# Kernel tuning notes

Hardware: AMD Instinct MI355X
Metric: run time of the kernel (lower is better)

Reference implementation:

```python
import jax, jax.numpy as jnp
import numpy as np

N_NODES = 100000


def gcn_layer(x, src, dst, W, b, num_nodes):
    """PyG GCNConv: out = D^-1/2 (A + I) D^-1/2 (x W) + b, with self-loops."""
    h = x @ W  # [N, out_dim]
    # add self-loops
    loop = jnp.arange(num_nodes, dtype=src.dtype)
    s = jnp.concatenate([src, loop])
    d = jnp.concatenate([dst, loop])
    # symmetric normalization (degree counted on destination, incl. self-loops)
    deg = jax.ops.segment_sum(jnp.ones_like(d, dtype=h.dtype), d, num_segments=num_nodes)
    dinv = jnp.where(deg > 0, jax.lax.rsqrt(deg), 0.0)
    norm = dinv[s] * dinv[d]  # [E+N]
    # gather -> weight -> scatter-add
    msg = h[s] * norm[:, None]  # [E+N, out_dim]
    out = jax.ops.segment_sum(msg, d, num_segments=num_nodes)
    return out + b


def setup_inputs() -> dict:
    key = jax.random.key(0)
    k1, k2, k3, k4 = jax.random.split(key, 4)
    in_chan, h1, h2 = 256, 128, 64
    n_edges = 1600000
    x = jax.random.normal(k1, (N_NODES, in_chan), dtype=jnp.float32)
    edge_index = jax.random.randint(k2, (2, n_edges), 0, N_NODES, dtype=jnp.int64)
    W1 = jax.random.normal(k3, (in_chan, h1), dtype=jnp.float32) * (1.0 / np.sqrt(in_chan))
    b1 = jnp.zeros((h1,), dtype=jnp.float32)
    W2 = jax.random.normal(k4, (h1, h2), dtype=jnp.float32) * (1.0 / np.sqrt(h1))
    b2 = jnp.zeros((h2,), dtype=jnp.float32)
    return {"x": x, "edge_index": edge_index, "W1": W1, "b1": b1, "W2": W2, "b2": b2}


def reference(x, edge_index, W1, b1, W2, b2):
    src, dst = edge_index[0], edge_index[1]
    h = jax.nn.relu(gcn_layer(x, src, dst, W1, b1, N_NODES))
    return jax.nn.relu(gcn_layer(h, src, dst, W2, b2, N_NODES))
```

## Files before the change

### kernel.cpp

```cpp
#include <hip/hip_runtime.h>
#include <hip/hip_fp16.h>

#define NNODES 100000

#define OFF_W1TH     0UL
#define OFF_W1TL     65536UL
#define OFF_W2TH     131072UL
#define OFF_W2TL     147456UL
#define OFF_BCNT     163840UL
#define OFF_BBASE    165888UL
#define OFF_BCUR     167936UL
#define OFF_ROWPTR   400128UL
#define OFF_DINV     1200640UL
#define OFF_COL      1605632UL
#define OFF_EBUF     8005632UL
#define OFF_H1G      8005632UL
#define OFF_H1OUT    59205632UL

typedef __attribute__((ext_vector_type(8))) _Float16 f16x8;
typedef __attribute__((ext_vector_type(4))) float f32x4;

__device__ __forceinline__ void async_copy16(void* lds, const void* g) {
    __builtin_amdgcn_global_load_lds(
        (const __attribute__((address_space(1))) unsigned*)g,
        (__attribute__((address_space(3))) unsigned*)lds, 16, 0, 0);
}

__global__ __launch_bounds__(256) void bincount(const int* __restrict__ dst,
                                                int* __restrict__ bcnt, int E) {
    __shared__ int lc[512];
    int t = threadIdx.x;
    lc[t] = 0; lc[t + 256] = 0;
    __syncthreads();
    for (int e = blockIdx.x * 256 + t; e < E; e += gridDim.x * 256)
        atomicAdd(&lc[dst[e] >> 8], 1);
    __syncthreads();
    if (lc[t]) atomicAdd(&bcnt[t], lc[t]);
    if (lc[t + 256]) atomicAdd(&bcnt[t + 256], lc[t + 256]);
}

__global__ __launch_bounds__(512) void bscan(const int* __restrict__ bcnt,
                                             int* __restrict__ bbase,
                                             int* __restrict__ bcur,
                                             int* __restrict__ rowptr,
                                             int NB, int N, int E) {
    __shared__ int s[512];
    int t = threadIdx.x;
    int v = (t < NB) ? bcnt[t] : 0;
    s[t] = v;
    __syncthreads();
    for (int off = 1; off < 512; off <<= 1) {
        int add = (t >= off) ? s[t - off] : 0;
        __syncthreads();
        s[t] += add;
        __syncthreads();
    }
    if (t < NB) {
        int ex = s[t] - v;
        bbase[t] = ex;
        bcur[t] = ex;
    }
    if (t == 0) rowptr[N] = E;
}

#define CHUNK 8192
__global__ __launch_bounds__(256) void binscatter(const int* __restrict__ src,
                                                  const int* __restrict__ dst,
                                                  int* __restrict__ bcur,
                                                  int* __restrict__ ebuf, int E) {
    __shared__ int lc[512];
    __shared__ int gb[512];
    int t = threadIdx.x;
    lc[t] = 0; lc[t + 256] = 0;
    __syncthreads();
    int base = blockIdx.x * CHUNK;
    int rb[32];
#pragma unroll
    for (int i = 0; i < 32; ++i) {
        int e = base + i * 256 + t;
        if (e < E) {
            int b = dst[e] >> 8;
            rb[i] = (b << 13) | atomicAdd(&lc[b], 1);
        } else rb[i] = -1;
    }
    __syncthreads();
    if (lc[t]) gb[t] = atomicAdd(&bcur[t], lc[t]);
    if (lc[t + 256]) gb[t + 256] = atomicAdd(&bcur[t + 256], lc[t + 256]);
    __syncthreads();
#pragma unroll
    for (int i = 0; i < 32; ++i) {
        if (rb[i] >= 0) {
            int e = base + i * 256 + t;
            int b = rb[i] >> 13, r = rb[i] & 8191;
            ebuf[gb[b] + r] = src[e] | ((dst[e] & 255) << 20);
        }
    }
}

__global__ __launch_bounds__(256) void buildcsr(const int* __restrict__ ebuf,
                                                const int* __restrict__ bbase,
                                                const int* __restrict__ bcnt,
                                                int* __restrict__ rowptr,
                                                int* __restrict__ colarr,
                                                float* __restrict__ dinv, int N) {
    int b = blockIdx.x;
    int t = threadIdx.x;
    int start = bbase[b];
    int cnt = bcnt[b];
    __shared__ int nc[256];
    __shared__ int s[256];
    __shared__ int ncur[256];
    nc[t] = 0;
    __syncthreads();
    for (int e = t; e < cnt; e += 256) atomicAdd(&nc[ebuf[start + e] >> 20], 1);
    __syncthreads();
    int own = nc[t];
    s[t] = own;
    __syncthreads();
    for (int off = 1; off < 256; off <<= 1) {
        int add = (t >= off) ? s[t - off] : 0;
        __syncthreads();
        s[t] += add;
        __syncthreads();
    }
    int rowbase = start + s[t] - own;
    int n0 = b << 8;
    if (n0 + t < N) {
        rowptr[n0 + t] = rowbase;
        dinv[n0 + t] = rsqrtf((float)(own + 1));
    }
    ncur[t] = rowbase;
    __syncthreads();
    for (int e = t; e < cnt; e += 256) {
        int pe = ebuf[start + e];
        int slot = atomicAdd(&ncur[pe >> 20], 1);
        colarr[slot] = pe & 0xFFFFF;
    }
}

__global__ __launch_bounds__(256) void split_wt_frag(const float* __restrict__ W,
                                                     _Float16* __restrict__ hi,
                                                     _Float16* __restrict__ lo,
                                                     int K, int N) {
    int idx = blockIdx.x * 256 + threadIdx.x;
    if (idx >= K * N) return;
    int NT = N >> 4;
    int j = idx & 7;
    int l = (idx >> 3) & 63;
    int f = idx >> 9;
    int nt = f % NT;
    int kc = f / NT;
    int k = kc * 32 + (l >> 4) * 8 + j;
    int n = nt * 16 + (l & 15);
    float v = W[k * N + n];
    _Float16 h = (_Float16)v;
    hi[idx] = h;
    lo[idx] = (_Float16)(v - (float)h);
}

template <int BN, int KTOT, bool AFP16>
__global__ __launch_bounds__(256, 3) void gemm_f16(const void* __restrict__ Araw,
                                                   const _Float16* __restrict__ Bh_g,
                                                   const _Float16* __restrict__ Bl_g,
                                                   const float* __restrict__ dinv,
                                                   _Float16* __restrict__ C, int M) {
    constexpr int NT = BN / 16;
    constexpr int FPW = (2 * NT) / 4;
    __shared__ _Float16 Ah[128][72];
    __shared__ _Float16 Bsh[2 * NT * 512];
    __shared__ _Float16 Bsl[2 * NT * 512];

    const int tid = threadIdx.x;
    const int wave = tid >> 6;
    const int lane = tid & 63;
    const int lm = lane & 15;
    const int q = lane >> 4;
    const int m0 = blockIdx.x * 128;

    f32x4 acc[2][NT];
#pragma unroll
    for (int a = 0; a < 2; ++a)
#pragma unroll
        for (int b = 0; b < NT; ++b) acc[a][b] = (f32x4){0.f, 0.f, 0.f, 0.f};

    for (int k0 = 0; k0 < KTOT; k0 += 64) {
        const int kc0 = k0 >> 5;
        const _Float16* bh_base = Bh_g + (size_t)kc0 * NT * 512;
        const _Float16* bl_base = Bl_g + (size_t)kc0 * NT * 512;
#pragma unroll
        for (int i = 0; i < FPW; ++i) {
            int f = wave * FPW + i;
            async_copy16(&Bsh[f * 512 + lane * 8], bh_base + f * 512 + lane * 8);
            async_copy16(&Bsl[f * 512 + lane * 8], bl_base + f * 512 + lane * 8);
        }
#pragma unroll
        for (int i = 0; i < 4; ++i) {
            int flat = tid + i * 256;
            int row = flat >> 3;
            int kk = (flat & 7) << 3;
            int gr = m0 + row;
            if (AFP16) {
                uint4 hv = make_uint4(0u, 0u, 0u, 0u);
                if (gr < M)
                    hv = *(const uint4*)&((const _Float16*)Araw)[(size_t)gr * KTOT + k0 + kk];
                *(uint4*)&Ah[row][kk] = hv;
            } else {
                const float* Af = (const float*)Araw;
                float4 v0 = make_float4(0.f, 0.f, 0.f, 0.f);
                float4 v1 = make_float4(0.f, 0.f, 0.f, 0.f);
                if (gr < M) {
                    v0 = *(const float4*)&Af[(size_t)gr * KTOT + k0 + kk];
                    v1 = *(const float4*)&Af[(size_t)gr * KTOT + k0 + kk + 4];
                }
                f16x8 h;
                h[0] = (_Float16)v0.x; h[1] = (_Float16)v0.y;
                h[2] = (_Float16)v0.z; h[3] = (_Float16)v0.w;
                h[4] = (_Float16)v1.x; h[5] = (_Float16)v1.y;
                h[6] = (_Float16)v1.z; h[7] = (_Float16)v1.w;
                *(f16x8*)&Ah[row][kk] = h;
            }
        }
        __syncthreads();

#pragma unroll
        for (int dkc = 0; dkc < 2; ++dkc) {
            f16x8 a[2];
#pragma unroll
            for (int mt = 0; mt < 2; ++mt)
                a[mt] = *(const f16x8*)&Ah[wave * 32 + mt * 16 + lm][dkc * 32 + q * 8];
#pragma unroll
            for (int nt = 0; nt < NT; ++nt) {
                f16x8 bh = *(const f16x8*)&Bsh[(dkc * NT + nt) * 512 + lane * 8];
                f16x8 bl = *(const f16x8*)&Bsl[(dkc * NT + nt) * 512 + lane * 8];
#pragma unroll
                for (int mt = 0; mt < 2; ++mt) {
                    acc[mt][nt] = __builtin_amdgcn_mfma_f32_16x16x32_f16(a[mt], bh, acc[mt][nt], 0, 0, 0);
                    acc[mt][nt] = __builtin_amdgcn_mfma_f32_16x16x32_f16(a[mt], bl, acc[mt][nt], 0, 0, 0);
                }
            }
        }
        __syncthreads();
    }

#pragma unroll
    for (int mt = 0; mt < 2; ++mt) {
#pragma unroll
        for (int i = 0; i < 4; ++i) {
            int r = m0 + wave * 32 + mt * 16 + q * 4 + i;
            if (r < M) {
                float dv = dinv[r];
#pragma unroll
                for (int nt = 0; nt < NT; ++nt) {
                    C[(size_t)r * BN + nt * 16 + lm] = (_Float16)(acc[mt][nt][i] * dv);
                }
            }
        }
    }
}

__device__ __forceinline__ void acc8(float* a, uint4 v) {
    float2 f0 = __half22float2(*(const __half2*)&v.x);
    float2 f1 = __half22float2(*(const __half2*)&v.y);
    float2 f2 = __half22float2(*(const __half2*)&v.z);
    float2 f3 = __half22float2(*(const __half2*)&v.w);
    a[0] += f0.x; a[1] += f0.y; a[2] += f1.x; a[3] += f1.y;
    a[4] += f2.x; a[5] += f2.y; a[6] += f3.x; a[7] += f3.y;
}

__global__ __launch_bounds__(256) void agg128(const _Float16* __restrict__ g,
                                              const int* __restrict__ rowptr,
                                              const int* __restrict__ colarr,
                                              const float* __restrict__ dinv,
                                              const float* __restrict__ bias,
                                              _Float16* __restrict__ out, int n) {
    int node = blockIdx.x * 4 + (threadIdx.x >> 6);
    int lane = threadIdx.x & 63;
    if (node >= n) return;
    int sel = lane >> 4;
    int co = (lane & 15) << 3;

    int beg = rowptr[node];
    int end = rowptr[node + 1];

    float a[8] = {0.f, 0.f, 0.f, 0.f, 0.f, 0.f, 0.f, 0.f};
    if (sel == 0) acc8(a, *(const uint4*)&g[(node << 7) + co]);

    int p = beg;
    for (; p + 16 <= end; p += 16) {
        int r0 = colarr[p + sel];
        int r1 = colarr[p + 4 + sel];
        int r2 = colarr[p + 8 + sel];
        int r3 = colarr[p + 12 + sel];
        uint4 v0 = *(const uint4*)&g[(r0 << 7) + co];
        uint4 v1 = *(const uint4*)&g[(r1 << 7) + co];
        uint4 v2 = *(const uint4*)&g[(r2 << 7) + co];
        uint4 v3 = *(const uint4*)&g[(r3 << 7) + co];
        acc8(a, v0); acc8(a, v1); acc8(a, v2); acc8(a, v3);
    }
    for (; p + 4 <= end; p += 4) {
        int r = colarr[p + sel];
        acc8(a, *(const uint4*)&g[(r << 7) + co]);
    }
    int rem = end - p;
    if (sel < rem) {
        int r = colarr[p + sel];
        acc8(a, *(const uint4*)&g[(r << 7) + co]);
    }

#pragma unroll
    for (int i = 0; i < 8; ++i) {
        a[i] += __shfl(a[i], lane ^ 16);
        a[i] += __shfl(a[i], lane ^ 32);
    }

    if (sel == 0) {
        float dv = dinv[node];
        float4 b0 = *(const float4*)&bias[co];
        float4 b1 = *(const float4*)&bias[co + 4];
        float o0 = fmaxf(fmaf(a[0], dv, b0.x), 0.f);
        float o1 = fmaxf(fmaf(a[1], dv, b0.y), 0.f);
        float o2 = fmaxf(fmaf(a[2], dv, b0.z), 0.f);
        float o3 = fmaxf(fmaf(a[3], dv, b0.w), 0.f);
        float o4 = fmaxf(fmaf(a[4], dv, b1.x), 0.f);
        float o5 = fmaxf(fmaf(a[5], dv, b1.y), 0.f);
        float o6 = fmaxf(fmaf(a[6], dv, b1.z), 0.f);
        float o7 = fmaxf(fmaf(a[7], dv, b1.w), 0.f);
        __half2 h0 = __floats2half2_rn(o0, o1);
        __half2 h1 = __floats2half2_rn(o2, o3);
        __half2 h2 = __floats2half2_rn(o4, o5);
        __half2 h3 = __floats2half2_rn(o6, o7);
        uint4 pk = make_uint4(*(unsigned*)&h0, *(unsigned*)&h1,
                              *(unsigned*)&h2, *(unsigned*)&h3);
        *(uint4*)&out[(node << 7) + co] = pk;
    }
}

__global__ __launch_bounds__(256) void agg64(const _Float16* __restrict__ g,
                                             const int* __restrict__ rowptr,
                                             const int* __restrict__ colarr,
                                             const float* __restrict__ dinv,
                                             const float* __restrict__ bias,
                                             float* __restrict__ out, int n) {
    int node = blockIdx.x * 4 + (threadIdx.x >> 6);
    int lane = threadIdx.x & 63;
    if (node >= n) return;
    int sel = lane >> 3;
    int co = (lane & 7) << 3;

    int beg = rowptr[node];
    int end = rowptr[node + 1];

    float a[8] = {0.f, 0.f, 0.f, 0.f, 0.f, 0.f, 0.f, 0.f};
    if (sel == 0) acc8(a, *(const uint4*)&g[(node << 6) + co]);

    int p = beg;
    for (; p + 16 <= end; p += 16) {
        int r0 = colarr[p + sel];
        int r1 = colarr[p + 8 + sel];
        uint4 v0 = *(const uint4*)&g[(r0 << 6) + co];
        uint4 v1 = *(const uint4*)&g[(r1 << 6) + co];
        acc8(a, v0); acc8(a, v1);
    }
    for (; p + 8 <= end; p += 8) {
        int r = colarr[p + sel];
        acc8(a, *(const uint4*)&g[(r << 6) + co]);
    }
    int rem = end - p;
    if (sel < rem) {
        int r = colarr[p + sel];
        acc8(a, *(const uint4*)&g[(r << 6) + co]);
    }

#pragma unroll
    for (int i = 0; i < 8; ++i) {
        a[i] += __shfl(a[i], lane ^ 8);
        a[i] += __shfl(a[i], lane ^ 16);
        a[i] += __shfl(a[i], lane ^ 32);
    }

    if (sel == 0) {
        float dv = dinv[node];
        float4 b0 = *(const float4*)&bias[co];
        float4 b1 = *(const float4*)&bias[co + 4];
        float4 oA, oB;
        oA.x = fmaxf(fmaf(a[0], dv, b0.x), 0.f);
        oA.y = fmaxf(fmaf(a[1], dv, b0.y), 0.f);
        oA.z = fmaxf(fmaf(a[2], dv, b0.z), 0.f);
        oA.w = fmaxf(fmaf(a[3], dv, b0.w), 0.f);
        oB.x = fmaxf(fmaf(a[4], dv, b1.x), 0.f);
        oB.y = fmaxf(fmaf(a[5], dv, b1.y), 0.f);
        oB.z = fmaxf(fmaf(a[6], dv, b1.z), 0.f);
        oB.w = fmaxf(fmaf(a[7], dv, b1.w), 0.f);
        *(float4*)&out[(node << 6) + co] = oA;
        *(float4*)&out[(node << 6) + co + 4] = oB;
    }
}

extern "C" void kernel_launch(void* const* d_in, const int* in_sizes, int n_in,
                              void* d_out, int out_size, void* d_ws, size_t ws_size,
                              hipStream_t stream) {
    const float* x  = (const float*)d_in[0];
    const int*   ei = (const int*)d_in[1];
    const float* W1 = (const float*)d_in[2];
    const float* b1 = (const float*)d_in[3];
    const float* W2 = (const float*)d_in[4];
    const float* b2 = (const float*)d_in[5];
    float* out = (float*)d_out;

    const int E = in_sizes[1] / 2;
    const int H1 = in_sizes[3];
    const int K1 = in_sizes[2] / H1;
    const int N = in_sizes[0] / K1;
    const int H2 = in_sizes[4] / H1;
    const int* src = ei;
    const int* dst = ei + E;
    const int NB = (N + 255) >> 8;

    char* ws = (char*)d_ws;
    _Float16* w1th   = (_Float16*)(ws + OFF_W1TH);
    _Float16* w1tl   = (_Float16*)(ws + OFF_W1TL);
    _Float16* w2th   = (_Float16*)(ws + OFF_W2TH);
    _Float16* w2tl   = (_Float16*)(ws + OFF_W2TL);
    int*      bcnt   = (int*)(ws + OFF_BCNT);
    int*      bbase  = (int*)(ws + OFF_BBASE);
    int*      bcur   = (int*)(ws + OFF_BCUR);
    int*      rowptr = (int*)(ws + OFF_ROWPTR);
    float*    dinv   = (float*)(ws + OFF_DINV);
    int*      colarr = (int*)(ws + OFF_COL);
    int*      ebuf   = (int*)(ws + OFF_EBUF);
    _Float16* h1g    = (_Float16*)(ws + OFF_H1G);
    _Float16* h1out  = (_Float16*)(ws + OFF_H1OUT);
    _Float16* h2g    = (_Float16*)(ws + OFF_H1G);

    hipMemsetAsync(bcnt, 0, 512 * sizeof(int), stream);
    bincount<<<256, 256, 0, stream>>>(dst, bcnt, E);
    bscan<<<1, 512, 0, stream>>>(bcnt, bbase, bcur, rowptr, NB, N, E);
    binscatter<<<(E + CHUNK - 1) / CHUNK, 256, 0, stream>>>(src, dst, bcur, ebuf, E);
    buildcsr<<<NB, 256, 0, stream>>>(ebuf, bbase, bcnt, rowptr, colarr, dinv, N);

    split_wt_frag<<<(K1 * H1 + 255) / 256, 256, 0, stream>>>(W1, w1th, w1tl, K1, H1);
    split_wt_frag<<<(H1 * H2 + 255) / 256, 256, 0, stream>>>(W2, w2th, w2tl, H1, H2);

    gemm_f16<128, 256, false><<<(N + 127) / 128, 256, 0, stream>>>(x, w1th, w1tl, dinv, h1g, N);
    agg128<<<(N + 3) / 4, 256, 0, stream>>>(h1g, rowptr, colarr, dinv, b1, h1out, N);

    gemm_f16<64, 128, true><<<(N + 127) / 128, 256, 0, stream>>>(h1out, w2th, w2tl, dinv, h2g, N);
    agg64<<<(N + 3) / 4, 256, 0, stream>>>(h2g, rowptr, colarr, dinv, b2, out, N);
}
```

Before: 372.7 us.

## Double-buffer B tiles and load A fragments directly into registers in GEMM

Restructures the dense GEMM so the split-fp16 weight tiles are double-buffered in LDS with async copies for the next K chunk issued before the current chunk's MFMAs. The A operand is no longer staged through LDS. Each lane loads its own fragment straight from global memory into registers, prefetched one chunk ahead. Launch bounds are raised to 4 blocks per CU. This removes the LDS round-trip and one barrier per step and overlaps loads with math, but lanes now read A in scattered 16/32-byte pieces with less coalescing, and register pressure goes up.

```diff
diff --git a/kernel.cpp b/kernel.cpp
--- a/kernel.cpp
+++ b/kernel.cpp
@@ -159,16 +159,17 @@
 }
 
 template <int BN, int KTOT, bool AFP16>
-__global__ __launch_bounds__(256, 3) void gemm_f16(const void* __restrict__ Araw,
+__global__ __launch_bounds__(256, 4) void gemm_f16(const void* __restrict__ Araw,
                                                    const _Float16* __restrict__ Bh_g,
                                                    const _Float16* __restrict__ Bl_g,
                                                    const float* __restrict__ dinv,
                                                    _Float16* __restrict__ C, int M) {
     constexpr int NT = BN / 16;
-    constexpr int FPW = (2 * NT) / 4;
-    __shared__ _Float16 Ah[128][72];
-    __shared__ _Float16 Bsh[2 * NT * 512];
-    __shared__ _Float16 Bsl[2 * NT * 512];
+    constexpr int NK = KTOT / 32;
+    constexpr int TILE = NT * 512;
+    constexpr int FPW = NT / 4;
+    __shared__ _Float16 Bsh[2][TILE];
+    __shared__ _Float16 Bsl[2][TILE];
 
     const int tid = threadIdx.x;
     const int wave = tid >> 6;
@@ -177,70 +178,90 @@
     const int q = lane >> 4;
     const int m0 = blockIdx.x * 128;
 
+    const int r0 = m0 + wave * 32 + lm;
+    const int r1 = r0 + 16;
+    const bool vr0 = r0 < M;
+    const bool vr1 = r1 < M;
+
+    const float* Af = (const float*)Araw;
+    const _Float16* Ah16 = (const _Float16*)Araw;
+
     f32x4 acc[2][NT];
 #pragma unroll
     for (int a = 0; a < 2; ++a)
 #pragma unroll
         for (int b = 0; b < NT; ++b) acc[a][b] = (f32x4){0.f, 0.f, 0.f, 0.f};
 
-    for (int k0 = 0; k0 < KTOT; k0 += 64) {
-        const int kc0 = k0 >> 5;
-        const _Float16* bh_base = Bh_g + (size_t)kc0 * NT * 512;
-        const _Float16* bl_base = Bl_g + (size_t)kc0 * NT * 512;
-#pragma unroll
-        for (int i = 0; i < FPW; ++i) {
-            int f = wave * FPW + i;
-            async_copy16(&Bsh[f * 512 + lane * 8], bh_base + f * 512 + lane * 8);
-            async_copy16(&Bsl[f * 512 + lane * 8], bl_base + f * 512 + lane * 8);
+    float4 pa0, pa1, pa2, pa3;
+    uint4 ph0, ph1;
+
+#define STAGE_B(kc_, b_)                                                          \
+    do {                                                                          \
+        _Pragma("unroll")                                                         \
+        for (int i_ = 0; i_ < FPW; ++i_) {                                        \
+            int f_ = wave * FPW + i_;                                             \
+            async_copy16(&Bsh[b_][f_ * 512 + lane * 8],                           \
+                         Bh_g + (size_t)(kc_) * TILE + f_ * 512 + lane * 8);      \
+            async_copy16(&Bsl[b_][f_ * 512 + lane * 8],                           \
+                         Bl_g + (size_t)(kc_) * TILE + f_ * 512 + lane * 8);      \
+        }                                                                         \
+    } while (0)
+
+#define LOAD_A(t_)                                                                \
+    do {                                                                          \
+        const int k_ = (t_) * 32 + q * 8;                                         \
+        if (AFP16) {                                                              \
+            ph0 = vr0 ? *(const uint4*)&Ah16[(size_t)r0 * KTOT + k_]              \
+                      : make_uint4(0u, 0u, 0u, 0u);                               \
+            ph1 = vr1 ? *(const uint4*)&Ah16[(size_t)r1 * KTOT + k_]              \
+                      : make_uint4(0u, 0u, 0u, 0u);                               \
+        } else {                                                                  \
+            float4 z_ = make_float4(0.f, 0.f, 0.f, 0.f);                          \
+            pa0 = vr0 ? *(const float4*)&Af[(size_t)r0 * KTOT + k_] : z_;         \
+            pa1 = vr0 ? *(const float4*)&Af[(size_t)r0 * KTOT + k_ + 4] : z_;     \
+            pa2 = vr1 ? *(const float4*)&Af[(size_t)r1 * KTOT + k_] : z_;         \
+            pa3 = vr1 ? *(const float4*)&Af[(size_t)r1 * KTOT + k_ + 4] : z_;     \
+        }                                                                         \
+    } while (0)
+
+    STAGE_B(0, 0);
+    LOAD_A(0);
+    __syncthreads();
+
+#pragma unroll
+    for (int t = 0; t < NK; ++t) {
+        const int b = t & 1;
+        if (t + 1 < NK) STAGE_B(t + 1, b ^ 1);
+
+        f16x8 a0, a1;
+        if (AFP16) {
+            a0 = *(f16x8*)&ph0;
+            a1 = *(f16x8*)&ph1;
+        } else {
+            a0[0] = (_Float16)pa0.x; a0[1] = (_Float16)pa0.y;
+            a0[2] = (_Float16)pa0.z; a0[3] = (_Float16)pa0.w;
+            a0[4] = (_Float16)pa1.x; a0[5] = (_Float16)pa1.y;
+            a0[6] = (_Float16)pa1.z; a0[7] = (_Float16)pa1.w;
+            a1[0] = (_Float16)pa2.x; a1[1] = (_Float16)pa2.y;
+            a1[2] = (_Float16)pa2.z; a1[3] = (_Float16)pa2.w;
+            a1[4] = (_Float16)pa3.x; a1[5] = (_Float16)pa3.y;
+            a1[6] = (_Float16)pa3.z; a1[7] = (_Float16)pa3.w;
         }
-#pragma unroll
-        for (int i = 0; i < 4; ++i) {
-            int flat = tid + i * 256;
-            int row = flat >> 3;
-            int kk = (flat & 7) << 3;
-            int gr = m0 + row;
-            if (AFP16) {
-                uint4 hv = make_uint4(0u, 0u, 0u, 0u);
-                if (gr < M)
-                    hv = *(const uint4*)&((const _Float16*)Araw)[(size_t)gr * KTOT + k0 + kk];
-                *(uint4*)&Ah[row][kk] = hv;
-            } else {
-                const float* Af = (const float*)Araw;
-                float4 v0 = make_float4(0.f, 0.f, 0.f, 0.f);
-                float4 v1 = make_float4(0.f, 0.f, 0.f, 0.f);
-                if (gr < M) {
-                    v0 = *(const float4*)&Af[(size_t)gr * KTOT + k0 + kk];
-                    v1 = *(const float4*)&Af[(size_t)gr * KTOT + k0 + kk + 4];
-                }
-                f16x8 h;
-                h[0] = (_Float16)v0.x; h[1] = (_Float16)v0.y;
-                h[2] = (_Float16)v0.z; h[3] = (_Float16)v0.w;
-                h[4] = (_Float16)v1.x; h[5] = (_Float16)v1.y;
-                h[6] = (_Float16)v1.z; h[7] = (_Float16)v1.w;
-                *(f16x8*)&Ah[row][kk] = h;
-            }
+        if (t + 1 < NK) LOAD_A(t + 1);
+
+#pragma unroll
+        for (int nt = 0; nt < NT; ++nt) {
+            f16x8 bh = *(const f16x8*)&Bsh[b][nt * 512 + lane * 8];
+            f16x8 bl = *(const f16x8*)&Bsl[b][nt * 512 + lane * 8];
+            acc[0][nt] = __builtin_amdgcn_mfma_f32_16x16x32_f16(a0, bh, acc[0][nt], 0, 0, 0);
+            acc[0][nt] = __builtin_amdgcn_mfma_f32_16x16x32_f16(a0, bl, acc[0][nt], 0, 0, 0);
+            acc[1][nt] = __builtin_amdgcn_mfma_f32_16x16x32_f16(a1, bh, acc[1][nt], 0, 0, 0);
+            acc[1][nt] = __builtin_amdgcn_mfma_f32_16x16x32_f16(a1, bl, acc[1][nt], 0, 0, 0);
         }
-        __syncthreads();
-
-#pragma unroll
-        for (int dkc = 0; dkc < 2; ++dkc) {
-            f16x8 a[2];
-#pragma unroll
-            for (int mt = 0; mt < 2; ++mt)
-                a[mt] = *(const f16x8*)&Ah[wave * 32 + mt * 16 + lm][dkc * 32 + q * 8];
-#pragma unroll
-            for (int nt = 0; nt < NT; ++nt) {
-                f16x8 bh = *(const f16x8*)&Bsh[(dkc * NT + nt) * 512 + lane * 8];
-                f16x8 bl = *(const f16x8*)&Bsl[(dkc * NT + nt) * 512 + lane * 8];
-#pragma unroll
-                for (int mt = 0; mt < 2; ++mt) {
-                    acc[mt][nt] = __builtin_amdgcn_mfma_f32_16x16x32_f16(a[mt], bh, acc[mt][nt], 0, 0, 0);
-                    acc[mt][nt] = __builtin_amdgcn_mfma_f32_16x16x32_f16(a[mt], bl, acc[mt][nt], 0, 0, 0);
-                }
-            }
-        }
-        __syncthreads();
-    }
+        if (t + 1 < NK) __syncthreads();
+    }
+#undef STAGE_B
+#undef LOAD_A
 
 #pragma unroll
     for (int mt = 0; mt < 2; ++mt) {
```

Result: slower. 417.5 us (+12.0%).

## Double-buffer A tile in GEMM with register prefetch of next K phase

Applied to the files above, without the earlier changes.

The GEMM now loads the next 64-wide K slice of A into registers while MFMAs run on the current slice, then converts it into a second LDS buffer. The K loop is fully unrolled and launch bounds drop from 3 to 2 blocks per SM to make room for the extra registers and LDS. The goal is to hide global load latency behind compute. The cost is lower occupancy and an extra barrier per phase around the B staging, since B stays single-buffered.

```diff
diff --git a/kernel.cpp b/kernel.cpp
--- a/kernel.cpp
+++ b/kernel.cpp
@@ -159,14 +159,15 @@
 }
 
 template <int BN, int KTOT, bool AFP16>
-__global__ __launch_bounds__(256, 3) void gemm_f16(const void* __restrict__ Araw,
+__global__ __launch_bounds__(256, 2) void gemm_f16(const void* __restrict__ Araw,
                                                    const _Float16* __restrict__ Bh_g,
                                                    const _Float16* __restrict__ Bl_g,
                                                    const float* __restrict__ dinv,
                                                    _Float16* __restrict__ C, int M) {
     constexpr int NT = BN / 16;
+    constexpr int NPH = KTOT / 64;
     constexpr int FPW = (2 * NT) / 4;
-    __shared__ _Float16 Ah[128][72];
+    __shared__ _Float16 Ah[2][128][72];
     __shared__ _Float16 Bsh[2 * NT * 512];
     __shared__ _Float16 Bsl[2 * NT * 512];
 
@@ -177,57 +178,92 @@
     const int q = lane >> 4;
     const int m0 = blockIdx.x * 128;
 
+    const float* Af = (const float*)Araw;
+    const _Float16* Ah16 = (const _Float16*)Araw;
+
     f32x4 acc[2][NT];
 #pragma unroll
     for (int a = 0; a < 2; ++a)
 #pragma unroll
         for (int b = 0; b < NT; ++b) acc[a][b] = (f32x4){0.f, 0.f, 0.f, 0.f};
 
-    for (int k0 = 0; k0 < KTOT; k0 += 64) {
-        const int kc0 = k0 >> 5;
-        const _Float16* bh_base = Bh_g + (size_t)kc0 * NT * 512;
-        const _Float16* bl_base = Bl_g + (size_t)kc0 * NT * 512;
-#pragma unroll
-        for (int i = 0; i < FPW; ++i) {
-            int f = wave * FPW + i;
-            async_copy16(&Bsh[f * 512 + lane * 8], bh_base + f * 512 + lane * 8);
-            async_copy16(&Bsl[f * 512 + lane * 8], bl_base + f * 512 + lane * 8);
-        }
-#pragma unroll
-        for (int i = 0; i < 4; ++i) {
-            int flat = tid + i * 256;
-            int row = flat >> 3;
-            int kk = (flat & 7) << 3;
-            int gr = m0 + row;
-            if (AFP16) {
-                uint4 hv = make_uint4(0u, 0u, 0u, 0u);
-                if (gr < M)
-                    hv = *(const uint4*)&((const _Float16*)Araw)[(size_t)gr * KTOT + k0 + kk];
-                *(uint4*)&Ah[row][kk] = hv;
-            } else {
-                const float* Af = (const float*)Araw;
-                float4 v0 = make_float4(0.f, 0.f, 0.f, 0.f);
-                float4 v1 = make_float4(0.f, 0.f, 0.f, 0.f);
-                if (gr < M) {
-                    v0 = *(const float4*)&Af[(size_t)gr * KTOT + k0 + kk];
-                    v1 = *(const float4*)&Af[(size_t)gr * KTOT + k0 + kk + 4];
-                }
-                f16x8 h;
-                h[0] = (_Float16)v0.x; h[1] = (_Float16)v0.y;
-                h[2] = (_Float16)v0.z; h[3] = (_Float16)v0.w;
-                h[4] = (_Float16)v1.x; h[5] = (_Float16)v1.y;
-                h[6] = (_Float16)v1.z; h[7] = (_Float16)v1.w;
-                *(f16x8*)&Ah[row][kk] = h;
-            }
-        }
-        __syncthreads();
+    const float4 fz_ = make_float4(0.f, 0.f, 0.f, 0.f);
+    const uint4 uz_ = make_uint4(0u, 0u, 0u, 0u);
+
+    float4 va[4][2];
+    uint4 ua[4];
+
+#define AISSUE(t_)                                                                \
+    do {                                                                          \
+        _Pragma("unroll")                                                         \
+        for (int i = 0; i < 4; ++i) {                                             \
+            int flat = tid + i * 256;                                             \
+            int row = flat >> 3;                                                  \
+            int kk = (flat & 7) << 3;                                             \
+            int gr = m0 + row;                                                    \
+            int gk = (t_) * 64 + kk;                                              \
+            if (AFP16) {                                                          \
+                ua[i] = (gr < M) ? *(const uint4*)&Ah16[(size_t)gr * KTOT + gk]   \
+                                 : uz_;                                           \
+            } else {                                                              \
+                va[i][0] = (gr < M) ? *(const float4*)&Af[(size_t)gr * KTOT + gk] \
+                                    : fz_;                                        \
+                va[i][1] = (gr < M)                                               \
+                               ? *(const float4*)&Af[(size_t)gr * KTOT + gk + 4]  \
+                               : fz_;                                             \
+            }                                                                     \
+        }                                                                         \
+    } while (0)
+
+#define ACVT(buf_)                                                                \
+    do {                                                                          \
+        _Pragma("unroll")                                                         \
+        for (int i = 0; i < 4; ++i) {                                             \
+            int flat = tid + i * 256;                                             \
+            int row = flat >> 3;                                                  \
+            int kk = (flat & 7) << 3;                                             \
+            if (AFP16) {                                                          \
+                *(uint4*)&Ah[buf_][row][kk] = ua[i];                              \
+            } else {                                                              \
+                f16x8 h;                                                          \
+                h[0] = (_Float16)va[i][0].x; h[1] = (_Float16)va[i][0].y;         \
+                h[2] = (_Float16)va[i][0].z; h[3] = (_Float16)va[i][0].w;         \
+                h[4] = (_Float16)va[i][1].x; h[5] = (_Float16)va[i][1].y;         \
+                h[6] = (_Float16)va[i][1].z; h[7] = (_Float16)va[i][1].w;         \
+                *(f16x8*)&Ah[buf_][row][kk] = h;                                  \
+            }                                                                     \
+        }                                                                         \
+    } while (0)
+
+#define STAGE_B(t_)                                                               \
+    do {                                                                          \
+        const int kc0_ = (t_) * 2;                                                \
+        const _Float16* bh_ = Bh_g + (size_t)kc0_ * NT * 512;                     \
+        const _Float16* bl_ = Bl_g + (size_t)kc0_ * NT * 512;                     \
+        _Pragma("unroll")                                                         \
+        for (int i = 0; i < FPW; ++i) {                                           \
+            int f_ = wave * FPW + i;                                              \
+            async_copy16(&Bsh[f_ * 512 + lane * 8], bh_ + f_ * 512 + lane * 8);   \
+            async_copy16(&Bsl[f_ * 512 + lane * 8], bl_ + f_ * 512 + lane * 8);   \
+        }                                                                         \
+    } while (0)
+
+    AISSUE(0);
+    ACVT(0);
+    STAGE_B(0);
+    __syncthreads();
+
+    int cur = 0;
+#pragma unroll
+    for (int t = 0; t < NPH; ++t) {
+        if (t + 1 < NPH) AISSUE(t + 1);
 
 #pragma unroll
         for (int dkc = 0; dkc < 2; ++dkc) {
             f16x8 a[2];
 #pragma unroll
             for (int mt = 0; mt < 2; ++mt)
-                a[mt] = *(const f16x8*)&Ah[wave * 32 + mt * 16 + lm][dkc * 32 + q * 8];
+                a[mt] = *(const f16x8*)&Ah[cur][wave * 32 + mt * 16 + lm][dkc * 32 + q * 8];
 #pragma unroll
             for (int nt = 0; nt < NT; ++nt) {
                 f16x8 bh = *(const f16x8*)&Bsh[(dkc * NT + nt) * 512 + lane * 8];
@@ -239,8 +275,18 @@
                 }
             }
         }
-        __syncthreads();
-    }
+
+        if (t + 1 < NPH) {
+            ACVT(cur ^ 1);
+            __syncthreads();
+            STAGE_B(t + 1);
+            __syncthreads();
+            cur ^= 1;
+        }
+    }
+#undef AISSUE
+#undef ACVT
+#undef STAGE_B
 
 #pragma unroll
     for (int mt = 0; mt < 2; ++mt) {
```

New measurement: 424.0 us. +13.8%, slower.

## Stage full A tile once and double-buffer B weight tiles in GEMM

Applied to the files above, without the earlier changes.

The GEMM now loads the whole 128-row A tile across all of K into LDS up front, with a padded stride, instead of reloading per 64-wide K step. The fp16 hi/lo weight tiles are double-buffered, so the next phase's async copy overlaps the current phase's MFMAs, and the per-step barriers drop to one per phase. The occupancy hint of 3 is removed from launch bounds. LDS use grows considerably, which may lower occupancy on the 256-wide K layer.

```diff
diff --git a/kernel.cpp b/kernel.cpp
--- a/kernel.cpp
+++ b/kernel.cpp
@@ -159,16 +159,21 @@
 }
 
 template <int BN, int KTOT, bool AFP16>
-__global__ __launch_bounds__(256, 3) void gemm_f16(const void* __restrict__ Araw,
-                                                   const _Float16* __restrict__ Bh_g,
-                                                   const _Float16* __restrict__ Bl_g,
-                                                   const float* __restrict__ dinv,
-                                                   _Float16* __restrict__ C, int M) {
+__global__ __launch_bounds__(256) void gemm_f16(const void* __restrict__ Araw,
+                                                const _Float16* __restrict__ Bh_g,
+                                                const _Float16* __restrict__ Bl_g,
+                                                const float* __restrict__ dinv,
+                                                _Float16* __restrict__ C, int M) {
     constexpr int NT = BN / 16;
-    constexpr int FPW = (2 * NT) / 4;
-    __shared__ _Float16 Ah[128][72];
-    __shared__ _Float16 Bsh[2 * NT * 512];
-    __shared__ _Float16 Bsl[2 * NT * 512];
+    constexpr int NKC = KTOT / 32;
+    constexpr int KCPP = AFP16 ? NKC : 2;
+    constexpr int NPH = NKC / KCPP;
+    constexpr int KPAD = KTOT + 8;
+    constexpr int BTILE = KCPP * NT * 512;
+    constexpr int NBUF = (NPH > 1) ? 2 : 1;
+    __shared__ _Float16 Ah[128 * KPAD];
+    __shared__ _Float16 Bsh[NBUF * BTILE];
+    __shared__ _Float16 Bsl[NBUF * BTILE];
 
     const int tid = threadIdx.x;
     const int wave = tid >> 6;
@@ -177,61 +182,95 @@
     const int q = lane >> 4;
     const int m0 = blockIdx.x * 128;
 
+#define STAGE_B(ph_, b_)                                                          \
+    do {                                                                          \
+        _Pragma("unroll")                                                         \
+        for (int c_ = 0; c_ < 4; ++c_) {                                          \
+            int off_ = (c_ * 256 + tid) * 8;                                      \
+            async_copy16(&Bsh[(b_) * BTILE + off_],                               \
+                         Bh_g + (size_t)(ph_) * BTILE + off_);                    \
+            async_copy16(&Bsl[(b_) * BTILE + off_],                               \
+                         Bl_g + (size_t)(ph_) * BTILE + off_);                    \
+        }                                                                         \
+    } while (0)
+
+    STAGE_B(0, 0);
+
+    if (AFP16) {
+        const _Float16* A16 = (const _Float16*)Araw;
+        constexpr int TPR = KTOT / 32;
+        constexpr int NIT = (128 * TPR) / 256;
+#pragma unroll
+        for (int i = 0; i < NIT; ++i) {
+            int flat = i * 256 + tid;
+            int row = flat / TPR;
+            int c0 = (flat % TPR) * 32;
+            int gr = m0 + row;
+            uint4 u0 = make_uint4(0u,0u,0u,0u), u1 = u0, u2 = u0, u3 = u0;
+            if (gr < M) {
+                const uint4* p = (const uint4*)&A16[(size_t)gr * KTOT + c0];
+                u0 = p[0]; u1 = p[1]; u2 = p[2]; u3 = p[3];
+            }
+            uint4* d = (uint4*)&Ah[row * KPAD + c0];
+            d[0] = u0; d[1] = u1; d[2] = u2; d[3] = u3;
+        }
+    } else {
+        const float* Af = (const float*)Araw;
+        constexpr int TPR = KTOT / 32;
+        constexpr int NIT = (128 * TPR) / 256;
+#pragma unroll
+        for (int i = 0; i < NIT; ++i) {
+            int flat = i * 256 + tid;
+            int row = flat / TPR;
+            int c0 = (flat % TPR) * 32;
+            int gr = m0 + row;
+            float4 v0 = make_float4(0.f,0.f,0.f,0.f);
+            float4 v1 = v0, v2 = v0, v3 = v0, v4 = v0, v5 = v0, v6 = v0, v7 = v0;
+            if (gr < M) {
+                const float4* p = (const float4*)&Af[(size_t)gr * KTOT + c0];
+                v0 = p[0]; v1 = p[1]; v2 = p[2]; v3 = p[3];
+                v4 = p[4]; v5 = p[5]; v6 = p[6]; v7 = p[7];
+            }
+            f16x8 h0, h1, h2, h3;
+            h0[0]=(_Float16)v0.x; h0[1]=(_Float16)v0.y; h0[2]=(_Float16)v0.z; h0[3]=(_Float16)v0.w;
+            h0[4]=(_Float16)v1.x; h0[5]=(_Float16)v1.y; h0[6]=(_Float16)v1.z; h0[7]=(_Float16)v1.w;
+            h1[0]=(_Float16)v2.x; h1[1]=(_Float16)v2.y; h1[2]=(_Float16)v2.z; h1[3]=(_Float16)v2.w;
+            h1[4]=(_Float16)v3.x; h1[5]=(_Float16)v3.y; h1[6]=(_Float16)v3.z; h1[7]=(_Float16)v3.w;
+            h2[0]=(_Float16)v4.x; h2[1]=(_Float16)v4.y; h2[2]=(_Float16)v4.z; h2[3]=(_Float16)v4.w;
+            h2[4]=(_Float16)v5.x; h2[5]=(_Float16)v5.y; h2[6]=(_Float16)v5.z; h2[7]=(_Float16)v5.w;
+            h3[0]=(_Float16)v6.x; h3[1]=(_Float16)v6.y; h3[2]=(_Float16)v6.z; h3[3]=(_Float16)v6.w;
+            h3[4]=(_Float16)v7.x; h3[5]=(_Float16)v7.y; h3[6]=(_Float16)v7.z; h3[7]=(_Float16)v7.w;
+            _Float16* d = &Ah[row * KPAD + c0];
+            *(f16x8*)&d[0]  = h0;
+            *(f16x8*)&d[8]  = h1;
+            *(f16x8*)&d[16] = h2;
+            *(f16x8*)&d[24] = h3;
+        }
+    }
+    __syncthreads();
+
     f32x4 acc[2][NT];
 #pragma unroll
     for (int a = 0; a < 2; ++a)
 #pragma unroll
         for (int b = 0; b < NT; ++b) acc[a][b] = (f32x4){0.f, 0.f, 0.f, 0.f};
 
-    for (int k0 = 0; k0 < KTOT; k0 += 64) {
-        const int kc0 = k0 >> 5;
-        const _Float16* bh_base = Bh_g + (size_t)kc0 * NT * 512;
-        const _Float16* bl_base = Bl_g + (size_t)kc0 * NT * 512;
-#pragma unroll
-        for (int i = 0; i < FPW; ++i) {
-            int f = wave * FPW + i;
-            async_copy16(&Bsh[f * 512 + lane * 8], bh_base + f * 512 + lane * 8);
-            async_copy16(&Bsl[f * 512 + lane * 8], bl_base + f * 512 + lane * 8);
-        }
-#pragma unroll
-        for (int i = 0; i < 4; ++i) {
-            int flat = tid + i * 256;
-            int row = flat >> 3;
-            int kk = (flat & 7) << 3;
-            int gr = m0 + row;
-            if (AFP16) {
-                uint4 hv = make_uint4(0u, 0u, 0u, 0u);
-                if (gr < M)
-                    hv = *(const uint4*)&((const _Float16*)Araw)[(size_t)gr * KTOT + k0 + kk];
-                *(uint4*)&Ah[row][kk] = hv;
-            } else {
-                const float* Af = (const float*)Araw;
-                float4 v0 = make_float4(0.f, 0.f, 0.f, 0.f);
-                float4 v1 = make_float4(0.f, 0.f, 0.f, 0.f);
-                if (gr < M) {
-                    v0 = *(const float4*)&Af[(size_t)gr * KTOT + k0 + kk];
-                    v1 = *(const float4*)&Af[(size_t)gr * KTOT + k0 + kk + 4];
-                }
-                f16x8 h;
-                h[0] = (_Float16)v0.x; h[1] = (_Float16)v0.y;
-                h[2] = (_Float16)v0.z; h[3] = (_Float16)v0.w;
-                h[4] = (_Float16)v1.x; h[5] = (_Float16)v1.y;
-                h[6] = (_Float16)v1.z; h[7] = (_Float16)v1.w;
-                *(f16x8*)&Ah[row][kk] = h;
-            }
-        }
-        __syncthreads();
-
-#pragma unroll
-        for (int dkc = 0; dkc < 2; ++dkc) {
+    int bufo = 0;
+#pragma unroll
+    for (int ph = 0; ph < NPH; ++ph) {
+        if (NPH > 1 && ph + 1 < NPH) STAGE_B(ph + 1, bufo ^ 1);
+
+#pragma unroll
+        for (int dkc = 0; dkc < KCPP; ++dkc) {
+            const int kc = ph * KCPP + dkc;
             f16x8 a[2];
 #pragma unroll
             for (int mt = 0; mt < 2; ++mt)
-                a[mt] = *(const f16x8*)&Ah[wave * 32 + mt * 16 + lm][dkc * 32 + q * 8];
+                a[mt] = *(const f16x8*)&Ah[(wave * 32 + mt * 16 + lm) * KPAD + kc * 32 + q * 8];
 #pragma unroll
             for (int nt = 0; nt < NT; ++nt) {
-                f16x8 bh = *(const f16x8*)&Bsh[(dkc * NT + nt) * 512 + lane * 8];
-                f16x8 bl = *(const f16x8*)&Bsl[(dkc * NT + nt) * 512 + lane * 8];
+                f16x8 bh = *(const f16x8*)&Bsh[bufo * BTILE + (dkc * NT + nt) * 512 + lane * 8];
+                f16x8 bl = *(const f16x8*)&Bsl[bufo * BTILE + (dkc * NT + nt) * 512 + lane * 8];
 #pragma unroll
                 for (int mt = 0; mt < 2; ++mt) {
                     acc[mt][nt] = __builtin_amdgcn_mfma_f32_16x16x32_f16(a[mt], bh, acc[mt][nt], 0, 0, 0);
@@ -239,8 +278,12 @@
                 }
             }
         }
-        __syncthreads();
-    }
+        if (ph + 1 < NPH) {
+            __syncthreads();
+            bufo ^= 1;
+        }
+    }
+#undef STAGE_B
 
 #pragma unroll
     for (int mt = 0; mt < 2; ++mt) {
```

Measured after the change: 391.6 us. 5.1% more time.
